# Kernel tuning notes

Measured on AMD Instinct MI355X. Metric: run time of the kernel, lower is better.

The kernel has to match this reference:

```python
import jax, jax.numpy as jnp
import numpy as np

N, M, NB, NA, NT, T, U = 1024, 32, 1024, 1536, 2048, 6, 32

def _one_hot_bool(n, m):
    ids = (jnp.arange(n) * m) // n  # contiguous assignment of entities to molecules
    return (jax.nn.one_hot(ids, m, dtype=jnp.float32) > 0.5)

def setup_inputs() -> dict:
    key = jax.random.key(0)
    ks = jax.random.split(key, 32)
    nrm = lambda i, shape, s=1.0: jax.random.normal(ks[i], shape, dtype=jnp.float32) * s
    inp = {
        'h_v': nrm(0, (N, U)), 'h_e': nrm(1, (NB, U)), 'h_a': nrm(2, (NA, U)),
        'h_t': nrm(3, (NT, U)), 'h_u': nrm(4, (M, U)),
        'h_v_history': nrm(5, (N, T, U)), 'h_e_history': nrm(6, (NB, T, U)),
        'h_a_history': nrm(7, (NA, T, U)), 'h_t_history': nrm(8, (NT, T, U)),
        'h_u_history': nrm(9, (M, T, U)),
        'atom_in_mol': _one_hot_bool(N, M), 'bond_in_mol': _one_hot_bool(NB, M),
        'angle_in_mol': _one_hot_bool(NA, M), 'torsion_in_mol': _one_hot_bool(NT, M),
        'adjacency_map': nrm(10, (N, N)), 'coordinates': nrm(11, (N, 3), 3.0),
        # learned parameters
        'Wk': nrm(12, (U, U), 0.1), 'bk': jnp.zeros((U,), jnp.float32),
        'Wq': nrm(13, (U, U), 0.1), 'bq': jnp.zeros((U,), jnp.float32),
        'Wv0': nrm(14, (1, U), 0.1), 'bv0': jnp.zeros((U,), jnp.float32),
        'Wv1': nrm(15, (U, U), 0.1), 'bv1': jnp.zeros((U,), jnp.float32),
        'Wp0': nrm(16, (3 * U, U), 0.1), 'bp0': jnp.zeros((U,), jnp.float32),
        'Wp1': nrm(17, (U, 19), 0.1), 'bp1': jnp.zeros((19,), jnp.float32),
        'Wd0': nrm(18, (5 * T * U, 64), 0.1), 'bd0': jnp.zeros((64,), jnp.float32),
        'Wd1': nrm(19, (64, 64), 0.1), 'bd1': jnp.zeros((64,), jnp.float32),
        'Wd2': nrm(20, (64, 19), 0.1), 'bd2': jnp.zeros((19,), jnp.float32),
    }
    return inp

def reference(h_v, h_e, h_a, h_t, h_u, h_v_history, h_e_history, h_a_history,
              h_t_history, h_u_history, atom_in_mol, bond_in_mol, angle_in_mol,
              torsion_in_mol, adjacency_map, coordinates,
              Wk, bk, Wq, bq, Wv0, bv0, Wv1, bv1, Wp0, bp0, Wp1, bp1,
              Wd0, bd0, Wd1, bd1, Wd2, bd2):
    A = atom_in_mol.astype(jnp.float32)              # [N, M]
    per_mol_mask = A @ A.T                           # [N, N] block-diagonal 0/1
    # pairwise Euclidean distance matrix
    diff = coordinates[:, None, :] - coordinates[None, :, :]
    dist = jnp.sqrt(jnp.maximum(jnp.sum(diff * diff, -1), 1e-12))[..., None]  # [N, N, 1]
    mask3 = per_mol_mask[..., None]                  # [N, N, 1]
    v = mask3 * (jax.nn.elu(dist @ Wv0 + bv0) @ Wv1 + bv1)          # [N, N, U]
    k = mask3 * (h_v @ Wk + bk)[:, None, :]                          # [N, N, U]
    q = mask3 * (h_v @ Wq + bq)[None, :, :]                          # [N, N, U]
    h_pair = jnp.concatenate([k, q, v], axis=2)                      # [N, N, 3U]
    h_pair = jnp.sum(jax.nn.sigmoid(h_pair @ Wp0 + bp0) @ Wp1 + bp1, axis=0)  # [N, 19]
    h_pair = A.T @ h_pair                                            # [M, 19]
    # per-mol segment sums of histories (faithful to mask-multiply-reduce, as einsum)
    seg = lambda mask, hist: jnp.einsum('em,etu->mtu', mask.astype(jnp.float32), hist)
    h_v_bar = seg(atom_in_mol, h_v_history).reshape(M, T * U)
    h_e_bar = seg(bond_in_mol, h_e_history).reshape(M, T * U)
    h_a_bar = seg(angle_in_mol, h_a_history).reshape(M, T * U)
    h_t_bar = seg(torsion_in_mol, h_t_history).reshape(M, T * U)  # computed, unused (as in source)
    # ConcatenateThenFullyConnect((64,'sigmoid',64,19)); note h_a_bar passed twice per source
    x = jnp.concatenate([h_v_bar, h_e_bar, h_u_history.reshape(M, T * U), h_a_bar, h_a_bar], axis=1)
    y = (jax.nn.sigmoid(x @ Wd0 + bd0) @ Wd1 + bd1) @ Wd2 + bd2      # [M, 19]
    return y + h_pair
```

## Files before the change

### kernel.cpp

```cpp
#include <hip/hip_runtime.h>
#include <math.h>


__device__ __forceinline__ float sigmoidf_(float x) { return 1.0f / (1.0f + __expf(-x)); }

__global__ __launch_bounds__(256) void fused_kernel(
    const float* __restrict__ h_v,
    const float* __restrict__ coords,
    const float* __restrict__ Wk, const float* __restrict__ bk,
    const float* __restrict__ Wq, const float* __restrict__ bq,
    const float* __restrict__ Wv0, const float* __restrict__ bv0,
    const float* __restrict__ Wv1, const float* __restrict__ bv1,
    const float* __restrict__ Wp0, const float* __restrict__ bp0,
    const float* __restrict__ Wp1, const float* __restrict__ bp1,
    const float* __restrict__ hvh,
    const float* __restrict__ heh,
    const float* __restrict__ hah,
    const float* __restrict__ huh,
    const float* __restrict__ Wd0, const float* __restrict__ bd0,
    const float* __restrict__ Wd1, const float* __restrict__ bd1,
    const float* __restrict__ Wd2, const float* __restrict__ bd2,
    float* __restrict__ out)
{
    __shared__ float SH[3072];
    __shared__ float Ql[32 * 36];
    __shared__ float Kl[4 * 36];
    __shared__ float wv1l[1024];
    __shared__ float wp0l[3072];
    __shared__ float wp1l[608];
    __shared__ float cbl[32], wv0l[32], bv0l[32];
    __shared__ float cxl[32], cyl[32], czl[32];
    __shared__ float Gl[4 * 32];
    __shared__ float Gs[32];

    const int tid = threadIdx.x;
    const int b = blockIdx.x;

    if (b < 32) {
        float* x  = SH;
        float* hp = SH + 960;
        float* h0 = SH + 1216;
        float* h1 = SH + 1280;
        const int m = b;

        if (tid < 192) {
            float sv = 0.0f, se = 0.0f, sa = 0.0f;
            const float* pv = hvh + (size_t)(m * 32) * 192 + tid;
            const float* pe = heh + (size_t)(m * 32) * 192 + tid;
            const float* pa = hah + (size_t)(m * 48) * 192 + tid;
            #pragma unroll 8
            for (int e = 0; e < 32; ++e) sv += pv[e * 192];
            #pragma unroll 8
            for (int e = 0; e < 32; ++e) se += pe[e * 192];
            #pragma unroll 8
            for (int e = 0; e < 48; ++e) sa += pa[e * 192];
            x[tid]       = sv;
            x[192 + tid] = se;
            x[384 + tid] = huh[m * 192 + tid];
            x[576 + tid] = sa;
            x[768 + tid] = sa;
        }
        __syncthreads();

        {
            const int o = tid & 63, part = tid >> 6;
            const int k0 = part * 240;
            float ssum = 0.0f;
            #pragma unroll 8
            for (int k = k0; k < k0 + 240; ++k) ssum += x[k] * Wd0[k * 64 + o];
            hp[part * 64 + o] = ssum;
        }
        __syncthreads();
        if (tid < 64)
            h0[tid] = sigmoidf_(hp[tid] + hp[64 + tid] + hp[128 + tid] + hp[192 + tid] + bd0[tid]);
        __syncthreads();
        if (tid < 64) {
            float ssum = bd1[tid];
            #pragma unroll
            for (int k = 0; k < 64; ++k) ssum += h0[k] * Wd1[k * 64 + tid];
            h1[tid] = ssum;
        }
        __syncthreads();
        if (tid < 19) {
            float y = bd2[tid];
            #pragma unroll
            for (int k = 0; k < 64; ++k) y += h1[k] * Wd2[k * 19 + tid];
            float c0m = 0.0f;
            for (int u = 0; u < 32; ++u) c0m += sigmoidf_(bp0[u]) * Wp1[u * 19 + tid];
            atomicAdd(&out[m * 19 + tid], y + 31744.0f * c0m + 32768.0f * bp1[tid]);
        }
        return;
    }

    const int bb = b - 32;
    const int mol = bb >> 3;
    const int oct = bb & 7;
    const int base = mol * 32;

    float* hl  = SH;
    float* wkl = SH + 1024;
    float* wql = SH + 2048;
    float* SQl = SH;
    float* W2l = SH + 1152;

    ((float4*)hl)[tid]   = ((const float4*)(h_v + (size_t)base * 32))[tid];
    ((float4*)wkl)[tid]  = ((const float4*)Wk)[tid];
    ((float4*)wql)[tid]  = ((const float4*)Wq)[tid];
    ((float4*)wv1l)[tid] = ((const float4*)Wv1)[tid];
    ((float4*)wp0l)[tid]       = ((const float4*)Wp0)[tid];
    ((float4*)wp0l)[tid + 256] = ((const float4*)Wp0)[tid + 256];
    ((float4*)wp0l)[tid + 512] = ((const float4*)Wp0)[tid + 512];
    for (int i = tid; i < 608; i += 256) wp1l[i] = Wp1[i];
    if (tid < 32) {
        wv0l[tid] = Wv0[tid];
        bv0l[tid] = bv0[tid];
        const int gi = base + tid;
        cxl[tid] = coords[gi * 3 + 0];
        cyl[tid] = coords[gi * 3 + 1];
        czl[tid] = coords[gi * 3 + 2];
    }
    __syncthreads();

    {
        const int u = tid & 31, g = tid >> 5;
        const int a0 = g * 4;
        float qa[4];
        #pragma unroll
        for (int j = 0; j < 4; ++j) qa[j] = bq[u];
        #pragma unroll
        for (int t4 = 0; t4 < 32; t4 += 4) {
            float4 h0 = *(const float4*)&hl[(a0 + 0) * 32 + t4];
            float4 h1 = *(const float4*)&hl[(a0 + 1) * 32 + t4];
            float4 h2 = *(const float4*)&hl[(a0 + 2) * 32 + t4];
            float4 h3 = *(const float4*)&hl[(a0 + 3) * 32 + t4];
            #pragma unroll
            for (int i = 0; i < 4; ++i) {
                const float wq = wql[(t4 + i) * 32 + u];
                qa[0] += (&h0.x)[i] * wq; qa[1] += (&h1.x)[i] * wq;
                qa[2] += (&h2.x)[i] * wq; qa[3] += (&h3.x)[i] * wq;
            }
        }
        #pragma unroll
        for (int j = 0; j < 4; ++j) Ql[(a0 + j) * 36 + u] = qa[j];

        if (g == oct) {
            float ka[4];
            #pragma unroll
            for (int j = 0; j < 4; ++j) ka[j] = bk[u];
            #pragma unroll
            for (int t4 = 0; t4 < 32; t4 += 4) {
                float4 h0 = *(const float4*)&hl[(a0 + 0) * 32 + t4];
                float4 h1 = *(const float4*)&hl[(a0 + 1) * 32 + t4];
                float4 h2 = *(const float4*)&hl[(a0 + 2) * 32 + t4];
                float4 h3 = *(const float4*)&hl[(a0 + 3) * 32 + t4];
                #pragma unroll
                for (int i = 0; i < 4; ++i) {
                    const float wk = wkl[(t4 + i) * 32 + u];
                    ka[0] += (&h0.x)[i] * wk; ka[1] += (&h1.x)[i] * wk;
                    ka[2] += (&h2.x)[i] * wk; ka[3] += (&h3.x)[i] * wk;
                }
            }
            #pragma unroll
            for (int j = 0; j < 4; ++j) Kl[j * 36 + u] = ka[j];
        }
    }
    __syncthreads();

    {
        const int w = tid & 31, g = tid >> 5;
        const int a0 = g * 4;
        float sq[4] = {0, 0, 0, 0}, w2[4] = {0, 0, 0, 0};
        #pragma unroll
        for (int u4 = 0; u4 < 32; u4 += 4) {
            float4 q0 = *(const float4*)&Ql[(a0 + 0) * 36 + u4];
            float4 q1 = *(const float4*)&Ql[(a0 + 1) * 36 + u4];
            float4 q2 = *(const float4*)&Ql[(a0 + 2) * 36 + u4];
            float4 q3 = *(const float4*)&Ql[(a0 + 3) * 36 + u4];
            float4 v0 = *(const float4*)&wv1l[(a0 + 0) * 32 + u4];
            float4 v1 = *(const float4*)&wv1l[(a0 + 1) * 32 + u4];
            float4 v2 = *(const float4*)&wv1l[(a0 + 2) * 32 + u4];
            float4 v3 = *(const float4*)&wv1l[(a0 + 3) * 32 + u4];
            #pragma unroll
            for (int i = 0; i < 4; ++i) {
                const float pq = wp0l[(32 + u4 + i) * 32 + w];
                const float pv = wp0l[(64 + u4 + i) * 32 + w];
                sq[0] += (&q0.x)[i] * pq; sq[1] += (&q1.x)[i] * pq;
                sq[2] += (&q2.x)[i] * pq; sq[3] += (&q3.x)[i] * pq;
                w2[0] += (&v0.x)[i] * pv; w2[1] += (&v1.x)[i] * pv;
                w2[2] += (&v2.x)[i] * pv; w2[3] += (&v3.x)[i] * pv;
            }
        }
        #pragma unroll
        for (int j = 0; j < 4; ++j) {
            SQl[(a0 + j) * 36 + w] = sq[j];
            W2l[(a0 + j) * 32 + w] = w2[j];
        }
        if (g == oct) {
            float sk[4] = {0, 0, 0, 0};
            #pragma unroll
            for (int u4 = 0; u4 < 32; u4 += 4) {
                float4 k0 = *(const float4*)&Kl[0 * 36 + u4];
                float4 k1 = *(const float4*)&Kl[1 * 36 + u4];
                float4 k2 = *(const float4*)&Kl[2 * 36 + u4];
                float4 k3 = *(const float4*)&Kl[3 * 36 + u4];
                #pragma unroll
                for (int i = 0; i < 4; ++i) {
                    const float pk = wp0l[(u4 + i) * 32 + w];
                    sk[0] += (&k0.x)[i] * pk; sk[1] += (&k1.x)[i] * pk;
                    sk[2] += (&k2.x)[i] * pk; sk[3] += (&k3.x)[i] * pk;
                }
            }
            #pragma unroll
            for (int j = 0; j < 4; ++j) Kl[j * 36 + w] = sk[j];
        }
    }
    if (tid < 32) {
        float s = bp0[tid];
        #pragma unroll
        for (int u = 0; u < 32; ++u) s += bv1[u] * wp0l[(64 + u) * 32 + tid];
        cbl[tid] = s;
    }
    __syncthreads();

    const int ps = tid >> 2, sub = tid & 3;
    const int p0 = oct * 128 + ps * 2;
    const int il = p0 >> 5;
    const int lil = ps >> 4;
    const int jl0 = p0 & 31, jl1 = jl0 + 1;

    const float cix = cxl[il], ciy = cyl[il], ciz = czl[il];
    const float dx0 = cix - cxl[jl0], dy0 = ciy - cyl[jl0], dz0 = ciz - czl[jl0];
    const float dx1 = cix - cxl[jl1], dy1 = ciy - cyl[jl1], dz1 = ciz - czl[jl1];
    const float dist0 = sqrtf(fmaxf(dx0 * dx0 + dy0 * dy0 + dz0 * dz0, 1e-12f));
    const float dist1 = sqrtf(fmaxf(dx1 * dx1 + dy1 * dy1 + dz1 * dz1, 1e-12f));

    float e0[32], e1[32];
    #pragma unroll
    for (int t = 0; t < 32; ++t) {
        const float x0 = dist0 * wv0l[t] + bv0l[t];
        const float x1 = dist1 * wv0l[t] + bv0l[t];
        e0[t] = (x0 > 0.0f) ? x0 : (__expf(x0) - 1.0f);
        e1[t] = (x1 > 0.0f) ? x1 : (__expf(x1) - 1.0f);
    }

    float s0[8], s1[8];
    {
        const float4 ska = *(const float4*)&Kl[lil * 36 + sub * 8];
        const float4 skb = *(const float4*)&Kl[lil * 36 + sub * 8 + 4];
        const float4 cba = *(const float4*)&cbl[sub * 8];
        const float4 cbb = *(const float4*)&cbl[sub * 8 + 4];
        const float4 q0a = *(const float4*)&SQl[jl0 * 36 + sub * 8];
        const float4 q0b = *(const float4*)&SQl[jl0 * 36 + sub * 8 + 4];
        const float4 q1a = *(const float4*)&SQl[jl1 * 36 + sub * 8];
        const float4 q1b = *(const float4*)&SQl[jl1 * 36 + sub * 8 + 4];
        #pragma unroll
        for (int i = 0; i < 4; ++i) {
            s0[i]     = (&ska.x)[i] + (&q0a.x)[i] + (&cba.x)[i];
            s0[i + 4] = (&skb.x)[i] + (&q0b.x)[i] + (&cbb.x)[i];
            s1[i]     = (&ska.x)[i] + (&q1a.x)[i] + (&cba.x)[i];
            s1[i + 4] = (&skb.x)[i] + (&q1b.x)[i] + (&cbb.x)[i];
        }
    }
    #pragma unroll
    for (int t = 0; t < 32; ++t) {
        const float4 wa = *(const float4*)&W2l[t * 32 + sub * 8];
        const float4 wb = *(const float4*)&W2l[t * 32 + sub * 8 + 4];
        const float a0 = e0[t], a1 = e1[t];
        #pragma unroll
        for (int i = 0; i < 4; ++i) {
            s0[i]     += a0 * (&wa.x)[i];
            s0[i + 4] += a0 * (&wb.x)[i];
            s1[i]     += a1 * (&wa.x)[i];
            s1[i + 4] += a1 * (&wb.x)[i];
        }
    }

    float g[8];
    #pragma unroll
    for (int k = 0; k < 8; ++k) g[k] = sigmoidf_(s0[k]) + sigmoidf_(s1[k]);
    #pragma unroll
    for (int k = 0; k < 8; ++k) {
        g[k] += __shfl_xor(g[k], 4);
        g[k] += __shfl_xor(g[k], 8);
        g[k] += __shfl_xor(g[k], 16);
        g[k] += __shfl_xor(g[k], 32);
    }
    const int lane = tid & 63, wid = tid >> 6;
    if (lane < 4) {
        #pragma unroll
        for (int k = 0; k < 8; ++k) Gl[wid * 32 + sub * 8 + k] = g[k];
    }
    __syncthreads();
    if (tid < 32) Gs[tid] = Gl[tid] + Gl[32 + tid] + Gl[64 + tid] + Gl[96 + tid];
    __syncthreads();
    if (tid < 19) {
        float r = 0.0f;
        #pragma unroll
        for (int u = 0; u < 32; ++u) r += Gs[u] * wp1l[u * 19 + tid];
        atomicAdd(&out[mol * 19 + tid], r);
    }
}

extern "C" void kernel_launch(void* const* d_in, const int* in_sizes, int n_in,
                              void* d_out, int out_size, void* d_ws, size_t ws_size,
                              hipStream_t stream) {
    (void)in_sizes; (void)n_in; (void)d_ws; (void)ws_size;
    const float* h_v    = (const float*)d_in[0];
    const float* hvh    = (const float*)d_in[5];
    const float* heh    = (const float*)d_in[6];
    const float* hah    = (const float*)d_in[7];
    const float* huh    = (const float*)d_in[9];
    const float* coords = (const float*)d_in[15];
    const float* Wk  = (const float*)d_in[16]; const float* bk  = (const float*)d_in[17];
    const float* Wq  = (const float*)d_in[18]; const float* bq  = (const float*)d_in[19];
    const float* Wv0 = (const float*)d_in[20]; const float* bv0 = (const float*)d_in[21];
    const float* Wv1 = (const float*)d_in[22]; const float* bv1 = (const float*)d_in[23];
    const float* Wp0 = (const float*)d_in[24]; const float* bp0 = (const float*)d_in[25];
    const float* Wp1 = (const float*)d_in[26]; const float* bp1 = (const float*)d_in[27];
    const float* Wd0 = (const float*)d_in[28]; const float* bd0 = (const float*)d_in[29];
    const float* Wd1 = (const float*)d_in[30]; const float* bd1 = (const float*)d_in[31];
    const float* Wd2 = (const float*)d_in[32]; const float* bd2 = (const float*)d_in[33];

    hipMemsetAsync(d_out, 0, (size_t)out_size * sizeof(float), stream);
    fused_kernel<<<288, 256, 0, stream>>>(h_v, coords, Wk, bk, Wq, bq,
                                          Wv0, bv0, Wv1, bv1, Wp0, bp0, Wp1, bp1,
                                          hvh, heh, hah, huh,
                                          Wd0, bd0, Wd1, bd1, Wd2, bd2,
                                          (float*)d_out);
}
```

Measured before the change: 21.63 us.

## Precompose K/Q/V weights with Wp0 in a prep kernel, drop memset

Adds a single-block prep kernel that multiplies Wk, Wq and Wv1 by their slices of Wp0, folds the biases into per-column constants, writes everything to workspace, and zeroes the output in place of the memset. The main kernel then projects h_v straight through the precomposed weights, removing the second 32x32 matmul stage and its barrier in each of the 256 pair blocks. This trades one extra dependent kernel launch for less per-block work and a smaller weight load into LDS.

```diff
diff --git a/kernel.cpp b/kernel.cpp
--- a/kernel.cpp
+++ b/kernel.cpp
@@ -2,17 +2,91 @@
 #include <math.h>
 
 
+#define WS_WK 0
+#define WS_WQ 1024
+#define WS_W2 2048
+#define WS_CK 3072
+#define WS_CQ 3104
+#define WS_CB 3136
+
 __device__ __forceinline__ float sigmoidf_(float x) { return 1.0f / (1.0f + __expf(-x)); }
+
+__global__ __launch_bounds__(256) void prep_kernel(
+    const float* __restrict__ Wk, const float* __restrict__ bk,
+    const float* __restrict__ Wq, const float* __restrict__ bq,
+    const float* __restrict__ Wv1, const float* __restrict__ bv1,
+    const float* __restrict__ Wp0, const float* __restrict__ bp0,
+    float* __restrict__ ws, float* __restrict__ out)
+{
+    __shared__ float wkl[1024], wql[1024], wv1l[1024], wp0l[3072];
+    const int tid = threadIdx.x;
+    ((float4*)wkl)[tid]  = ((const float4*)Wk)[tid];
+    ((float4*)wql)[tid]  = ((const float4*)Wq)[tid];
+    ((float4*)wv1l)[tid] = ((const float4*)Wv1)[tid];
+    ((float4*)wp0l)[tid]       = ((const float4*)Wp0)[tid];
+    ((float4*)wp0l)[tid + 256] = ((const float4*)Wp0)[tid + 256];
+    ((float4*)wp0l)[tid + 512] = ((const float4*)Wp0)[tid + 512];
+    out[tid] = 0.0f;
+    if (tid + 256 < 608) out[tid + 256] = 0.0f;
+    if (tid + 512 < 608) out[tid + 512] = 0.0f;
+    __syncthreads();
+
+    const int w = tid & 31, g = tid >> 5;
+    const int a0 = g * 4;
+    float k_[4] = {0, 0, 0, 0}, q_[4] = {0, 0, 0, 0}, v_[4] = {0, 0, 0, 0};
+    #pragma unroll
+    for (int u4 = 0; u4 < 32; u4 += 4) {
+        float4 k0 = *(const float4*)&wkl[(a0 + 0) * 32 + u4];
+        float4 k1 = *(const float4*)&wkl[(a0 + 1) * 32 + u4];
+        float4 k2 = *(const float4*)&wkl[(a0 + 2) * 32 + u4];
+        float4 k3 = *(const float4*)&wkl[(a0 + 3) * 32 + u4];
+        float4 q0 = *(const float4*)&wql[(a0 + 0) * 32 + u4];
+        float4 q1 = *(const float4*)&wql[(a0 + 1) * 32 + u4];
+        float4 q2 = *(const float4*)&wql[(a0 + 2) * 32 + u4];
+        float4 q3 = *(const float4*)&wql[(a0 + 3) * 32 + u4];
+        float4 v0 = *(const float4*)&wv1l[(a0 + 0) * 32 + u4];
+        float4 v1 = *(const float4*)&wv1l[(a0 + 1) * 32 + u4];
+        float4 v2 = *(const float4*)&wv1l[(a0 + 2) * 32 + u4];
+        float4 v3 = *(const float4*)&wv1l[(a0 + 3) * 32 + u4];
+        #pragma unroll
+        for (int i = 0; i < 4; ++i) {
+            const float pk = wp0l[(u4 + i) * 32 + w];
+            const float pq = wp0l[(32 + u4 + i) * 32 + w];
+            const float pv = wp0l[(64 + u4 + i) * 32 + w];
+            k_[0] += (&k0.x)[i] * pk; k_[1] += (&k1.x)[i] * pk;
+            k_[2] += (&k2.x)[i] * pk; k_[3] += (&k3.x)[i] * pk;
+            q_[0] += (&q0.x)[i] * pq; q_[1] += (&q1.x)[i] * pq;
+            q_[2] += (&q2.x)[i] * pq; q_[3] += (&q3.x)[i] * pq;
+            v_[0] += (&v0.x)[i] * pv; v_[1] += (&v1.x)[i] * pv;
+            v_[2] += (&v2.x)[i] * pv; v_[3] += (&v3.x)[i] * pv;
+        }
+    }
+    #pragma unroll
+    for (int j = 0; j < 4; ++j) {
+        ws[WS_WK + (a0 + j) * 32 + w] = k_[j];
+        ws[WS_WQ + (a0 + j) * 32 + w] = q_[j];
+        ws[WS_W2 + (a0 + j) * 32 + w] = v_[j];
+    }
+    if (tid < 32) {
+        float s1 = 0.0f, s2 = 0.0f, s3 = bp0[tid];
+        #pragma unroll
+        for (int u = 0; u < 32; ++u) {
+            s1 += bk[u]  * wp0l[u * 32 + tid];
+            s2 += bq[u]  * wp0l[(32 + u) * 32 + tid];
+            s3 += bv1[u] * wp0l[(64 + u) * 32 + tid];
+        }
+        ws[WS_CK + tid] = s1;
+        ws[WS_CQ + tid] = s2;
+        ws[WS_CB + tid] = s3;
+    }
+}
 
 __global__ __launch_bounds__(256) void fused_kernel(
     const float* __restrict__ h_v,
     const float* __restrict__ coords,
-    const float* __restrict__ Wk, const float* __restrict__ bk,
-    const float* __restrict__ Wq, const float* __restrict__ bq,
     const float* __restrict__ Wv0, const float* __restrict__ bv0,
-    const float* __restrict__ Wv1, const float* __restrict__ bv1,
-    const float* __restrict__ Wp0, const float* __restrict__ bp0,
     const float* __restrict__ Wp1, const float* __restrict__ bp1,
+    const float* __restrict__ bp0,
     const float* __restrict__ hvh,
     const float* __restrict__ heh,
     const float* __restrict__ hah,
@@ -20,15 +94,14 @@
     const float* __restrict__ Wd0, const float* __restrict__ bd0,
     const float* __restrict__ Wd1, const float* __restrict__ bd1,
     const float* __restrict__ Wd2, const float* __restrict__ bd2,
+    const float* __restrict__ ws,
     float* __restrict__ out)
 {
-    __shared__ float SH[3072];
-    __shared__ float Ql[32 * 36];
-    __shared__ float Kl[4 * 36];
-    __shared__ float wv1l[1024];
-    __shared__ float wp0l[3072];
+    __shared__ float SH[4096];
+    __shared__ float SQl[32 * 36];
+    __shared__ float SKl4[4 * 36];
     __shared__ float wp1l[608];
-    __shared__ float cbl[32], wv0l[32], bv0l[32];
+    __shared__ float ckl[32], cql[32], cbl[32], wv0l[32], bv0l[32];
     __shared__ float cxl[32], cyl[32], czl[32];
     __shared__ float Gl[4 * 32];
     __shared__ float Gs[32];
@@ -61,7 +134,6 @@
             x[768 + tid] = sa;
         }
         __syncthreads();
-
         {
             const int o = tid & 63, part = tid >> 6;
             const int k0 = part * 240;
@@ -98,20 +170,19 @@
     const int base = mol * 32;
 
     float* hl  = SH;
-    float* wkl = SH + 1024;
-    float* wql = SH + 2048;
-    float* SQl = SH;
-    float* W2l = SH + 1152;
-
-    ((float4*)hl)[tid]   = ((const float4*)(h_v + (size_t)base * 32))[tid];
-    ((float4*)wkl)[tid]  = ((const float4*)Wk)[tid];
-    ((float4*)wql)[tid]  = ((const float4*)Wq)[tid];
-    ((float4*)wv1l)[tid] = ((const float4*)Wv1)[tid];
-    ((float4*)wp0l)[tid]       = ((const float4*)Wp0)[tid];
-    ((float4*)wp0l)[tid + 256] = ((const float4*)Wp0)[tid + 256];
-    ((float4*)wp0l)[tid + 512] = ((const float4*)Wp0)[tid + 512];
+    float* WKl = SH + 1024;
+    float* WQl = SH + 2048;
+    float* W2l = SH + 3072;
+
+    ((float4*)hl)[tid]  = ((const float4*)(h_v + (size_t)base * 32))[tid];
+    ((float4*)WKl)[tid] = ((const float4*)(ws + WS_WK))[tid];
+    ((float4*)WQl)[tid] = ((const float4*)(ws + WS_WQ))[tid];
+    ((float4*)W2l)[tid] = ((const float4*)(ws + WS_W2))[tid];
     for (int i = tid; i < 608; i += 256) wp1l[i] = Wp1[i];
     if (tid < 32) {
+        ckl[tid] = ws[WS_CK + tid];
+        cql[tid] = ws[WS_CQ + tid];
+        cbl[tid] = ws[WS_CB + tid];
         wv0l[tid] = Wv0[tid];
         bv0l[tid] = bv0[tid];
         const int gi = base + tid;
@@ -126,99 +197,43 @@
         const int a0 = g * 4;
         float qa[4];
         #pragma unroll
-        for (int j = 0; j < 4; ++j) qa[j] = bq[u];
+        for (int j = 0; j < 4; ++j) qa[j] = cql[u];
         #pragma unroll
         for (int t4 = 0; t4 < 32; t4 += 4) {
-            float4 h0 = *(const float4*)&hl[(a0 + 0) * 32 + t4];
-            float4 h1 = *(const float4*)&hl[(a0 + 1) * 32 + t4];
-            float4 h2 = *(const float4*)&hl[(a0 + 2) * 32 + t4];
-            float4 h3 = *(const float4*)&hl[(a0 + 3) * 32 + t4];
+            float4 h0v = *(const float4*)&hl[(a0 + 0) * 32 + t4];
+            float4 h1v = *(const float4*)&hl[(a0 + 1) * 32 + t4];
+            float4 h2v = *(const float4*)&hl[(a0 + 2) * 32 + t4];
+            float4 h3v = *(const float4*)&hl[(a0 + 3) * 32 + t4];
             #pragma unroll
             for (int i = 0; i < 4; ++i) {
-                const float wq = wql[(t4 + i) * 32 + u];
-                qa[0] += (&h0.x)[i] * wq; qa[1] += (&h1.x)[i] * wq;
-                qa[2] += (&h2.x)[i] * wq; qa[3] += (&h3.x)[i] * wq;
+                const float wq = WQl[(t4 + i) * 32 + u];
+                qa[0] += (&h0v.x)[i] * wq; qa[1] += (&h1v.x)[i] * wq;
+                qa[2] += (&h2v.x)[i] * wq; qa[3] += (&h3v.x)[i] * wq;
             }
         }
         #pragma unroll
-        for (int j = 0; j < 4; ++j) Ql[(a0 + j) * 36 + u] = qa[j];
+        for (int j = 0; j < 4; ++j) SQl[(a0 + j) * 36 + u] = qa[j];
 
         if (g == oct) {
             float ka[4];
             #pragma unroll
-            for (int j = 0; j < 4; ++j) ka[j] = bk[u];
+            for (int j = 0; j < 4; ++j) ka[j] = ckl[u];
             #pragma unroll
             for (int t4 = 0; t4 < 32; t4 += 4) {
-                float4 h0 = *(const float4*)&hl[(a0 + 0) * 32 + t4];
-                float4 h1 = *(const float4*)&hl[(a0 + 1) * 32 + t4];
-                float4 h2 = *(const float4*)&hl[(a0 + 2) * 32 + t4];
-                float4 h3 = *(const float4*)&hl[(a0 + 3) * 32 + t4];
+                float4 h0v = *(const float4*)&hl[(a0 + 0) * 32 + t4];
+                float4 h1v = *(const float4*)&hl[(a0 + 1) * 32 + t4];
+                float4 h2v = *(const float4*)&hl[(a0 + 2) * 32 + t4];
+                float4 h3v = *(const float4*)&hl[(a0 + 3) * 32 + t4];
                 #pragma unroll
                 for (int i = 0; i < 4; ++i) {
-                    const float wk = wkl[(t4 + i) * 32 + u];
-                    ka[0] += (&h0.x)[i] * wk; ka[1] += (&h1.x)[i] * wk;
-                    ka[2] += (&h2.x)[i] * wk; ka[3] += (&h3.x)[i] * wk;
+                    const float wk = WKl[(t4 + i) * 32 + u];
+                    ka[0] += (&h0v.x)[i] * wk; ka[1] += (&h1v.x)[i] * wk;
+                    ka[2] += (&h2v.x)[i] * wk; ka[3] += (&h3v.x)[i] * wk;
                 }
             }
             #pragma unroll
-            for (int j = 0; j < 4; ++j) Kl[j * 36 + u] = ka[j];
-        }
-    }
-    __syncthreads();
-
-    {
-        const int w = tid & 31, g = tid >> 5;
-        const int a0 = g * 4;
-        float sq[4] = {0, 0, 0, 0}, w2[4] = {0, 0, 0, 0};
-        #pragma unroll
-        for (int u4 = 0; u4 < 32; u4 += 4) {
-            float4 q0 = *(const float4*)&Ql[(a0 + 0) * 36 + u4];
-            float4 q1 = *(const float4*)&Ql[(a0 + 1) * 36 + u4];
-            float4 q2 = *(const float4*)&Ql[(a0 + 2) * 36 + u4];
-            float4 q3 = *(const float4*)&Ql[(a0 + 3) * 36 + u4];
-            float4 v0 = *(const float4*)&wv1l[(a0 + 0) * 32 + u4];
-            float4 v1 = *(const float4*)&wv1l[(a0 + 1) * 32 + u4];
-            float4 v2 = *(const float4*)&wv1l[(a0 + 2) * 32 + u4];
-            float4 v3 = *(const float4*)&wv1l[(a0 + 3) * 32 + u4];
-            #pragma unroll
-            for (int i = 0; i < 4; ++i) {
-                const float pq = wp0l[(32 + u4 + i) * 32 + w];
-                const float pv = wp0l[(64 + u4 + i) * 32 + w];
-                sq[0] += (&q0.x)[i] * pq; sq[1] += (&q1.x)[i] * pq;
-                sq[2] += (&q2.x)[i] * pq; sq[3] += (&q3.x)[i] * pq;
-                w2[0] += (&v0.x)[i] * pv; w2[1] += (&v1.x)[i] * pv;
-                w2[2] += (&v2.x)[i] * pv; w2[3] += (&v3.x)[i] * pv;
-            }
-        }
-        #pragma unroll
-        for (int j = 0; j < 4; ++j) {
-            SQl[(a0 + j) * 36 + w] = sq[j];
-            W2l[(a0 + j) * 32 + w] = w2[j];
-        }
-        if (g == oct) {
-            float sk[4] = {0, 0, 0, 0};
-            #pragma unroll
-            for (int u4 = 0; u4 < 32; u4 += 4) {
-                float4 k0 = *(const float4*)&Kl[0 * 36 + u4];
-                float4 k1 = *(const float4*)&Kl[1 * 36 + u4];
-                float4 k2 = *(const float4*)&Kl[2 * 36 + u4];
-                float4 k3 = *(const float4*)&Kl[3 * 36 + u4];
-                #pragma unroll
-                for (int i = 0; i < 4; ++i) {
-                    const float pk = wp0l[(u4 + i) * 32 + w];
-                    sk[0] += (&k0.x)[i] * pk; sk[1] += (&k1.x)[i] * pk;
-                    sk[2] += (&k2.x)[i] * pk; sk[3] += (&k3.x)[i] * pk;
-                }
-            }
-            #pragma unroll
-            for (int j = 0; j < 4; ++j) Kl[j * 36 + w] = sk[j];
-        }
-    }
-    if (tid < 32) {
-        float s = bp0[tid];
-        #pragma unroll
-        for (int u = 0; u < 32; ++u) s += bv1[u] * wp0l[(64 + u) * 32 + tid];
-        cbl[tid] = s;
+            for (int j = 0; j < 4; ++j) SKl4[j * 36 + u] = ka[j];
+        }
     }
     __syncthreads();
 
@@ -245,8 +260,8 @@
 
     float s0[8], s1[8];
     {
-        const float4 ska = *(const float4*)&Kl[lil * 36 + sub * 8];
-        const float4 skb = *(const float4*)&Kl[lil * 36 + sub * 8 + 4];
+        const float4 ska = *(const float4*)&SKl4[lil * 36 + sub * 8];
+        const float4 skb = *(const float4*)&SKl4[lil * 36 + sub * 8 + 4];
         const float4 cba = *(const float4*)&cbl[sub * 8];
         const float4 cbb = *(const float4*)&cbl[sub * 8 + 4];
         const float4 q0a = *(const float4*)&SQl[jl0 * 36 + sub * 8];
@@ -304,7 +319,7 @@
 extern "C" void kernel_launch(void* const* d_in, const int* in_sizes, int n_in,
                               void* d_out, int out_size, void* d_ws, size_t ws_size,
                               hipStream_t stream) {
-    (void)in_sizes; (void)n_in; (void)d_ws; (void)ws_size;
+    (void)in_sizes; (void)n_in; (void)out_size; (void)ws_size;
     const float* h_v    = (const float*)d_in[0];
     const float* hvh    = (const float*)d_in[5];
     const float* heh    = (const float*)d_in[6];
@@ -321,10 +336,12 @@
     const float* Wd1 = (const float*)d_in[30]; const float* bd1 = (const float*)d_in[31];
     const float* Wd2 = (const float*)d_in[32]; const float* bd2 = (const float*)d_in[33];
 
-    hipMemsetAsync(d_out, 0, (size_t)out_size * sizeof(float), stream);
-    fused_kernel<<<288, 256, 0, stream>>>(h_v, coords, Wk, bk, Wq, bq,
-                                          Wv0, bv0, Wv1, bv1, Wp0, bp0, Wp1, bp1,
+    float* ws = (float*)d_ws;
+
+    prep_kernel<<<1, 256, 0, stream>>>(Wk, bk, Wq, bq, Wv1, bv1, Wp0, bp0,
+                                       ws, (float*)d_out);
+    fused_kernel<<<288, 256, 0, stream>>>(h_v, coords, Wv0, bv0, Wp1, bp1, bp0,
                                           hvh, heh, hah, huh,
                                           Wd0, bd0, Wd1, bd1, Wd2, bd2,
-                                          (float*)d_out);
+                                          ws, (float*)d_out);
 }
```

New measurement: 21.47 us. Within noise of the previous version (-0.8%).
